# Kernel optimization log

Measured on AMD Instinct MI355X. Metric: run time of the kernel, lower is better.

The kernel has to match this reference:

```python
import jax, jax.numpy as jnp
import numpy as np

N_NODES = 100000
N_EDGES = 1600000
IN_CH = 165


def setup_inputs() -> dict:
    key = jax.random.key(0)
    ks = jax.random.split(key, 6)
    x = jax.random.normal(ks[0], (N_NODES, IN_CH), dtype=jnp.float32)
    edge_index = jax.random.randint(ks[1], (2, N_EDGES), 0, N_NODES, dtype=jnp.int32)
    # Glorot-ish init for weights
    W1 = jax.random.normal(ks[2], (IN_CH, 128), dtype=jnp.float32) * (1.0 / np.sqrt(IN_CH))
    b1 = jnp.zeros((128,), dtype=jnp.float32)
    W2 = jax.random.normal(ks[3], (128, 64), dtype=jnp.float32) * (1.0 / np.sqrt(128))
    b2 = jnp.zeros((64,), dtype=jnp.float32)
    Wo = jax.random.normal(ks[4], (64, 2), dtype=jnp.float32) * (1.0 / np.sqrt(64))
    bo = jnp.zeros((2,), dtype=jnp.float32)
    return {"x": x, "edge_index": edge_index, "W1": W1, "b1": b1,
            "W2": W2, "b2": b2, "Wo": Wo, "bo": bo}


def _gcn_norm(edge_index, n_nodes, dtype):
    """Add self-loops and compute symmetric normalization deg^-1/2 * deg^-1/2 (PyG gcn_norm)."""
    loops = jnp.arange(n_nodes, dtype=edge_index.dtype)
    ei = jnp.concatenate([edge_index, jnp.stack([loops, loops])], axis=1)
    row, col = ei[0], ei[1]
    deg = jax.ops.segment_sum(jnp.ones(ei.shape[1], dtype), col, num_segments=n_nodes)
    deg_inv_sqrt = jnp.where(deg > 0, jax.lax.rsqrt(deg), 0.0)
    norm = deg_inv_sqrt[row] * deg_inv_sqrt[col]  # [E+N]
    return row, col, norm


def _gcn_conv(h, row, col, norm, W, b, n_nodes):
    # transform first (F_in -> F_out), then gather-scale-scatter aggregate
    m = h @ W                                   # [N, F_out]
    msg = m[row] * norm[:, None]                # [E+N, F_out]
    agg = jax.ops.segment_sum(msg, col, num_segments=n_nodes)
    return agg + b


def reference(x, edge_index, W1, b1, W2, b2, Wo, bo):
    n_nodes = x.shape[0]
    row, col, norm = _gcn_norm(edge_index, n_nodes, x.dtype)
    h = jax.nn.relu(_gcn_conv(x, row, col, norm, W1, b1, n_nodes))
    h = jax.nn.relu(_gcn_conv(h, row, col, norm, W2, b2, n_nodes))
    return h @ Wo + bo  # [N, 2] logits
```

## Files before the change

kernel.cpp:

```cpp
#include <hip/hip_runtime.h>

#define N_NODES 100000
#define N_EDGES 1600000
#define IN_CH   165
#define BSHIFT 7
#define NBUCK  ((N_NODES + 127) / 128)
#define BCAP   3072
#define PA_BLOCKS 196
#define WSPLIT_BLOCKS 128
#define G1_BLOCKS ((N_NODES + 63) / 64)

typedef unsigned short ushort_t;
typedef _Float16 f16;
typedef _Float16 f16x8 __attribute__((ext_vector_type(8)));
typedef _Float16 hfrag8 __attribute__((ext_vector_type(8)));
typedef short bfrag8 __attribute__((ext_vector_type(8)));
typedef float f32x4 __attribute__((ext_vector_type(4)));

__device__ __forceinline__ ushort_t f2bf(float f) {
    unsigned u = __float_as_uint(f);
    unsigned r = (u + 0x7fffu + ((u >> 16) & 1u)) >> 16;
    return (ushort_t)r;
}
__device__ __forceinline__ float bf2f(ushort_t h) {
    return __uint_as_float(((unsigned)h) << 16);
}

__device__ __forceinline__ void fmix_lo(float& a, unsigned pair, float s) {
    asm("v_fma_mix_f32 %0, %1, %2, %0 op_sel_hi:[1,0,0]" : "+v"(a) : "v"(pair), "v"(s));
}
__device__ __forceinline__ void fmix_hi(float& a, unsigned pair, float s) {
    asm("v_fma_mix_f32 %0, %1, %2, %0 op_sel:[1,0,0] op_sel_hi:[1,0,0]" : "+v"(a) : "v"(pair), "v"(s));
}
__device__ __forceinline__ void fmix_acc8(float* acc, uint4 v, float s) {
    fmix_lo(acc[0], v.x, s); fmix_hi(acc[1], v.x, s);
    fmix_lo(acc[2], v.y, s); fmix_hi(acc[3], v.y, s);
    fmix_lo(acc[4], v.z, s); fmix_hi(acc[5], v.z, s);
    fmix_lo(acc[6], v.w, s); fmix_hi(acc[7], v.w, s);
}

__global__ void bucketA_kernel(const int* __restrict__ row, const int* __restrict__ col,
                               int* __restrict__ bfill, unsigned* __restrict__ tmp,
                               const float* __restrict__ W1, const float* __restrict__ W2,
                               ushort_t* __restrict__ wt1h, ushort_t* __restrict__ wt1l,
                               ushort_t* __restrict__ wt2h, ushort_t* __restrict__ wt2l) {
    __shared__ int lcnt[NBUCK];
    __shared__ int lcur[NBUCK];
    int t = threadIdx.x;
    if (blockIdx.x >= PA_BLOCKS) {
        int i = (blockIdx.x - PA_BLOCKS) * 256 + t;
        if (i < 128 * 192) {
            int ch = i / 192, k = i - ch * 192;
            float v = (k < IN_CH) ? W1[(size_t)k * 128 + ch] : 0.f;
            ushort_t h = f2bf(v);
            wt1h[i] = h;
            wt1l[i] = f2bf(v - bf2f(h));
        } else if (i < 128 * 192 + 64 * 128) {
            int j = i - 128 * 192;
            int ch = j / 128, k = j - ch * 128;
            float v = W2[(size_t)k * 64 + ch];
            f16 h = (f16)v;
            f16 l = (f16)(v - (float)h);
            wt2h[j] = *(ushort_t*)&h;
            wt2l[j] = *(ushort_t*)&l;
        }
        return;
    }
    int e0 = (int)((long)blockIdx.x * N_EDGES / PA_BLOCKS);
    int e1 = (int)((long)(blockIdx.x + 1) * N_EDGES / PA_BLOCKS);
    for (int i = t; i < NBUCK; i += 256) lcnt[i] = 0;
    __syncthreads();
    for (int e = e0 + t; e < e1; e += 256)
        atomicAdd(&lcnt[col[e] >> BSHIFT], 1);
    __syncthreads();
    for (int b = t; b < NBUCK; b += 256) {
        int c = lcnt[b];
        lcur[b] = (c > 0) ? (b * BCAP + atomicAdd(&bfill[b], c)) : 0;
    }
    __syncthreads();
    for (int e = e0 + t; e < e1; e += 256) {
        int cc = col[e];
        int b = cc >> BSHIFT;
        int p = atomicAdd(&lcur[b], 1);
        tmp[p] = ((unsigned)(cc & 127) << 17) | (unsigned)row[e];
    }
}

__launch_bounds__(256)
__global__ void g1prep_kernel(const unsigned* __restrict__ tmp, const int* __restrict__ bfill,
                              int* __restrict__ cnt, int* __restrict__ bbase, int* __restrict__ off,
                              const float* __restrict__ X,
                              const ushort_t* __restrict__ wth, const ushort_t* __restrict__ wtl,
                              f16* __restrict__ M, int n_nodes) {
    __shared__ char smem[20480];
    int t = threadIdx.x;
    if (blockIdx.x < NBUCK) {
        int* lcnt = (int*)smem;
        int* ssc  = (int*)(smem + 512);
        int b = blockIdx.x;
        if (t < 128) lcnt[t] = 0;
        __syncthreads();
        int total = min(bfill[b], BCAP);
        const unsigned* reg = tmp + (size_t)b * BCAP;
        for (int i = t; i < total; i += 256)
            atomicAdd(&lcnt[(reg[i] >> 17) & 127], 1);
        __syncthreads();
        if (t < 128) {
            int n = (b << BSHIFT) + t;
            if (n < N_NODES) cnt[n] = lcnt[t];
        }
        if (b == 0) {
            int v[4]; int run = 0;
            int base = t * 4;
            #pragma unroll
            for (int j = 0; j < 4; ++j) {
                int c = (base + j < NBUCK) ? bfill[base + j] : 0;
                v[j] = run; run += c;
            }
            ssc[t] = run;
            __syncthreads();
            for (int o = 1; o < 256; o <<= 1) {
                int x = (t >= o) ? ssc[t - o] : 0;
                __syncthreads();
                ssc[t] += x;
                __syncthreads();
            }
            int prev = (t > 0) ? ssc[t - 1] : 0;
            #pragma unroll
            for (int j = 0; j < 4; ++j)
                if (base + j < NBUCK) bbase[base + j] = prev + v[j];
            if (t == 0) off[N_NODES] = N_EDGES;
        }
        return;
    }
    constexpr int XP = 40;
    ushort_t (*wsh)[XP] = (ushort_t(*)[XP])smem;
    ushort_t (*wsl)[XP] = (ushort_t(*)[XP])(smem + 10240);

    int bid = blockIdx.x - NBUCK;
    int l = t & 63, wid = t >> 6;
    long node0 = (long)bid * 64;
    int r = (int)node0 + wid * 16 + (l & 15);
    int rr = min(r, n_nodes - 1);
    int q = l >> 4;
    const float* xrow = X + (size_t)rr * IN_CH;

    f32x4 acc[8];
    #pragma unroll
    for (int ct = 0; ct < 8; ++ct) acc[ct] = (f32x4){0.f, 0.f, 0.f, 0.f};

    bfrag8 wfh[2], wfl[2];
    float a[8];

    auto loadW = [&](int c) {
        int k0 = c * 32;
        #pragma unroll
        for (int i = 0; i < 2; ++i) {
            int idx = t + i * 256;
            int ch = idx >> 2, qq = idx & 3;
            wfh[i] = *(const bfrag8*)&wth[(size_t)ch * 192 + k0 + qq * 8];
            wfl[i] = *(const bfrag8*)&wtl[(size_t)ch * 192 + k0 + qq * 8];
        }
    };
    auto storeW = [&]() {
        #pragma unroll
        for (int i = 0; i < 2; ++i) {
            int idx = t + i * 256;
            int ch = idx >> 2, qq = idx & 3;
            *(bfrag8*)&wsh[ch][qq * 8] = wfh[i];
            *(bfrag8*)&wsl[ch][qq * 8] = wfl[i];
        }
    };
    auto loadX = [&](int c) {
        int k = c * 32 + q * 8;
        if (c < 5) {
            #pragma unroll
            for (int i = 0; i < 8; ++i) a[i] = xrow[k + i];
        } else {
            #pragma unroll
            for (int i = 0; i < 8; ++i) a[i] = 0.f;
            if (q == 0) {
                a[0] = xrow[160]; a[1] = xrow[161]; a[2] = xrow[162];
                a[3] = xrow[163]; a[4] = xrow[164];
            }
        }
    };

    loadW(0);
    loadX(0);
    #pragma unroll 1
    for (int c = 0; c < 6; ++c) {
        storeW();
        __syncthreads();
        if (c + 1 < 6) loadW(c + 1);
        bfrag8 ah, al;
        #pragma unroll
        for (int i = 0; i < 8; ++i) {
            ushort_t h = (ushort_t)(__float_as_uint(a[i]) >> 16);
            ah[i] = (short)h;
            al[i] = (short)f2bf(a[i] - bf2f(h));
        }
        if (c + 1 < 6) loadX(c + 1);
        #pragma unroll
        for (int ct = 0; ct < 8; ++ct) {
            bfrag8 bh = *(const bfrag8*)&wsh[ct * 16 + (l & 15)][q * 8];
            bfrag8 bl = *(const bfrag8*)&wsl[ct * 16 + (l & 15)][q * 8];
            acc[ct] = __builtin_amdgcn_mfma_f32_16x16x32_bf16(ah, bh, acc[ct], 0, 0, 0);
            acc[ct] = __builtin_amdgcn_mfma_f32_16x16x32_bf16(ah, bl, acc[ct], 0, 0, 0);
            acc[ct] = __builtin_amdgcn_mfma_f32_16x16x32_bf16(al, bh, acc[ct], 0, 0, 0);
        }
        __syncthreads();
    }

    int nl = wid * 16 + (l >> 4) * 4;
    #pragma unroll
    for (int ct = 0; ct < 8; ++ct) {
        int ch = ct * 16 + (l & 15);
        #pragma unroll
        for (int j = 0; j < 4; ++j) {
            long node = node0 + nl + j;
            if (node < n_nodes)
                M[node * 128 + ch] = (f16)acc[ct][j];
        }
    }
}

__global__ void bucketB2_kernel(const unsigned* __restrict__ tmp, const int* __restrict__ bfill,
                                const int* __restrict__ bbase, const int* __restrict__ cnt,
                                int* __restrict__ off, unsigned* __restrict__ srt) {
    __shared__ int sh[128];
    __shared__ int lcur[128];
    int b = blockIdx.x, t = threadIdx.x;
    int nb0 = b << BSHIFT;
    int base = bbase[b];
    if (t < 128) {
        int n = nb0 + t;
        sh[t] = (n < N_NODES) ? cnt[n] : 0;
    }
    __syncthreads();
    for (int o = 1; o < 128; o <<= 1) {
        int x = (t < 128 && t >= o) ? sh[t - o] : 0;
        __syncthreads();
        if (t < 128) sh[t] += x;
        __syncthreads();
    }
    if (t < 128) {
        int excl = (t > 0) ? sh[t - 1] : 0;
        int n = nb0 + t;
        if (n < N_NODES) off[n] = base + excl;
        lcur[t] = excl;
    }
    __syncthreads();
    int total = min(bfill[b], BCAP);
    const unsigned* reg = tmp + (size_t)b * BCAP;
    for (int i = t; i < total; i += 256) {
        unsigned e = reg[i];
        int c = (e >> 17) & 127;
        unsigned src = e & 0x1FFFFu;
        unsigned cs = min((unsigned)cnt[src], 255u);
        int p = atomicAdd(&lcur[c], 1);
        srt[base + p] = (cs << 17) | src;
    }
}

__launch_bounds__(256)
__global__ void gemm2_kernel(const f16* __restrict__ H,
                             const ushort_t* __restrict__ wth, const ushort_t* __restrict__ wtl,
                             f16* __restrict__ M, int n_nodes) {
    constexpr int XP = 40;
    __shared__ ushort_t wsh[64][XP];
    __shared__ ushort_t wsl[64][XP];
    int t = threadIdx.x;
    int l = t & 63, wid = t >> 6;
    long node0 = (long)blockIdx.x * 64;
    int r = (int)node0 + wid * 16 + (l & 15);
    int rr = min(r, n_nodes - 1);
    int q = l >> 4;
    const f16* hrow = H + (size_t)rr * 128;

    f32x4 acc[4];
    #pragma unroll
    for (int ct = 0; ct < 4; ++ct) acc[ct] = (f32x4){0.f, 0.f, 0.f, 0.f};

    bfrag8 wfh, wfl;
    auto loadW = [&](int c) {
        int ch = t >> 2, qq = t & 3;
        wfh = *(const bfrag8*)&wth[(size_t)ch * 128 + c * 32 + qq * 8];
        wfl = *(const bfrag8*)&wtl[(size_t)ch * 128 + c * 32 + qq * 8];
    };
    auto storeW = [&]() {
        int ch = t >> 2, qq = t & 3;
        *(bfrag8*)&wsh[ch][qq * 8] = wfh;
        *(bfrag8*)&wsl[ch][qq * 8] = wfl;
    };

    loadW(0);
    hfrag8 a = *(const hfrag8*)&hrow[q * 8];
    #pragma unroll 1
    for (int c = 0; c < 4; ++c) {
        storeW();
        __syncthreads();
        if (c + 1 < 4) loadW(c + 1);
        hfrag8 acur = a;
        if (c + 1 < 4) a = *(const hfrag8*)&hrow[(c + 1) * 32 + q * 8];
        #pragma unroll
        for (int ct = 0; ct < 4; ++ct) {
            hfrag8 bh = *(const hfrag8*)&wsh[ct * 16 + (l & 15)][q * 8];
            hfrag8 bl = *(const hfrag8*)&wsl[ct * 16 + (l & 15)][q * 8];
            acc[ct] = __builtin_amdgcn_mfma_f32_16x16x32_f16(acur, bh, acc[ct], 0, 0, 0);
            acc[ct] = __builtin_amdgcn_mfma_f32_16x16x32_f16(acur, bl, acc[ct], 0, 0, 0);
        }
        __syncthreads();
    }

    int nl = wid * 16 + (l >> 4) * 4;
    #pragma unroll
    for (int ct = 0; ct < 4; ++ct) {
        int ch = ct * 16 + (l & 15);
        #pragma unroll
        for (int j = 0; j < 4; ++j) {
            long node = node0 + nl + j;
            if (node < n_nodes)
                M[node * 64 + ch] = (f16)acc[ct][j];
        }
    }
}

__global__ void agg1_kernel(const f16* __restrict__ ms, const unsigned* __restrict__ srt,
                            const int* __restrict__ off,
                            const float* __restrict__ b1, f16* __restrict__ h1) {
    int wave = threadIdx.x >> 6;
    int lane = threadIdx.x & 63;
    int n = blockIdx.x * 4 + wave;
    if (n >= N_NODES) return;
    int g = lane >> 4, p = lane & 15;
    const char* msb = (const char*)ms;
    unsigned pb = (unsigned)p * 16;
    int s0 = off[n], s1 = off[n + 1];
    float dn = rsqrtf((float)(s1 - s0) + 1.f);
    float acc[8] = {0.f, 0.f, 0.f, 0.f, 0.f, 0.f, 0.f, 0.f};
    if (g == 0) {
        uint4 v = *(const uint4*)(msb + (unsigned)n * 256 + pb);
        fmix_acc8(acc, v, dn);
    }
    unsigned sv = (s0 + lane < s1) ? srt[s0 + lane] : 0;
    for (int base = s0; base < s1; base += 64) {
        int nb2 = base + 64;
        unsigned svn = (nb2 + lane < s1) ? srt[nb2 + lane] : 0;
        int cnt_ = min(64, s1 - base);
        int j = 0;
        for (; j + 15 < cnt_; j += 16) {
            unsigned e0 = (unsigned)__shfl((int)sv, j + g);
            unsigned e1 = (unsigned)__shfl((int)sv, j + 4 + g);
            unsigned e2 = (unsigned)__shfl((int)sv, j + 8 + g);
            unsigned e3 = (unsigned)__shfl((int)sv, j + 12 + g);
            uint4 v0 = *(const uint4*)(msb + (e0 & 0x1FFFFu) * 256 + pb);
            uint4 v1 = *(const uint4*)(msb + (e1 & 0x1FFFFu) * 256 + pb);
            uint4 v2 = *(const uint4*)(msb + (e2 & 0x1FFFFu) * 256 + pb);
            uint4 v3 = *(const uint4*)(msb + (e3 & 0x1FFFFu) * 256 + pb);
            float d0 = rsqrtf((float)(e0 >> 17) + 1.f);
            float d1 = rsqrtf((float)(e1 >> 17) + 1.f);
            float d2 = rsqrtf((float)(e2 >> 17) + 1.f);
            float d3 = rsqrtf((float)(e3 >> 17) + 1.f);
            fmix_acc8(acc, v0, d0);
            fmix_acc8(acc, v1, d1);
            fmix_acc8(acc, v2, d2);
            fmix_acc8(acc, v3, d3);
        }
        for (; j < cnt_; j += 4) {
            unsigned e = (unsigned)__shfl((int)sv, j + g);
            float ws = (j + g < cnt_) ? rsqrtf((float)(e >> 17) + 1.f) : 0.f;
            uint4 v = *(const uint4*)(msb + (e & 0x1FFFFu) * 256 + pb);
            fmix_acc8(acc, v, ws);
        }
        sv = svn;
    }
    #pragma unroll
    for (int i = 0; i < 8; ++i) {
        acc[i] += __shfl_xor(acc[i], 16);
        acc[i] += __shfl_xor(acc[i], 32);
    }
    if (lane < 16) {
        float4 ba = ((const float4*)b1)[lane * 2];
        float4 bb = ((const float4*)b1)[lane * 2 + 1];
        float bv[8] = {ba.x, ba.y, ba.z, ba.w, bb.x, bb.y, bb.z, bb.w};
        f16x8 r;
        #pragma unroll
        for (int i = 0; i < 8; ++i)
            r[i] = (f16)fmaxf(acc[i] * dn + bv[i], 0.f);
        *(f16x8*)(h1 + (size_t)n * 128 + lane * 8) = r;
    }
}

__global__ void agg2_kernel(const f16* __restrict__ ms, const unsigned* __restrict__ srt,
                            const int* __restrict__ off,
                            const float* __restrict__ b2, const float* __restrict__ Wo,
                            const float* __restrict__ bo, float* __restrict__ out) {
    int wave = threadIdx.x >> 6;
    int lane = threadIdx.x & 63;
    int n = blockIdx.x * 4 + wave;
    if (n >= N_NODES) return;
    int g = lane >> 3, p = lane & 7;
    const char* msb = (const char*)ms;
    unsigned pb = (unsigned)p * 16;
    int s0 = off[n], s1 = off[n + 1];
    float dn = rsqrtf((float)(s1 - s0) + 1.f);
    float acc[8] = {0.f, 0.f, 0.f, 0.f, 0.f, 0.f, 0.f, 0.f};
    if (g == 0) {
        uint4 v = *(const uint4*)(msb + (unsigned)n * 128 + pb);
        fmix_acc8(acc, v, dn);
    }
    unsigned sv = (s0 + lane < s1) ? srt[s0 + lane] : 0;
    for (int base = s0; base < s1; base += 64) {
        int nb2 = base + 64;
        unsigned svn = (nb2 + lane < s1) ? srt[nb2 + lane] : 0;
        int cnt_ = min(64, s1 - base);
        int j = 0;
        for (; j + 15 < cnt_; j += 16) {
            unsigned e0 = (unsigned)__shfl((int)sv, j + g);
            unsigned e1 = (unsigned)__shfl((int)sv, j + 8 + g);
            uint4 v0 = *(const uint4*)(msb + (e0 & 0x1FFFFu) * 128 + pb);
            uint4 v1 = *(const uint4*)(msb + (e1 & 0x1FFFFu) * 128 + pb);
            float d0 = rsqrtf((float)(e0 >> 17) + 1.f);
            float d1 = rsqrtf((float)(e1 >> 17) + 1.f);
            fmix_acc8(acc, v0, d0);
            fmix_acc8(acc, v1, d1);
        }
        for (; j < cnt_; j += 8) {
            unsigned e = (unsigned)__shfl((int)sv, j + g);
            float ws = (j + g < cnt_) ? rsqrtf((float)(e >> 17) + 1.f) : 0.f;
            uint4 v = *(const uint4*)(msb + (e & 0x1FFFFu) * 128 + pb);
            fmix_acc8(acc, v, ws);
        }
        sv = svn;
    }
    #pragma unroll
    for (int i = 0; i < 8; ++i) {
        acc[i] += __shfl_xor(acc[i], 8);
        acc[i] += __shfl_xor(acc[i], 16);
        acc[i] += __shfl_xor(acc[i], 32);
    }
    float p0 = 0.f, p1 = 0.f;
    #pragma unroll
    for (int i = 0; i < 8; ++i) {
        int ch = p * 8 + i;
        float hc = fmaxf(acc[i] * dn + b2[ch], 0.f);
        p0 = fmaf(hc, Wo[ch * 2], p0);
        p1 = fmaf(hc, Wo[ch * 2 + 1], p1);
    }
    p0 += __shfl_xor(p0, 1); p1 += __shfl_xor(p1, 1);
    p0 += __shfl_xor(p0, 2); p1 += __shfl_xor(p1, 2);
    p0 += __shfl_xor(p0, 4); p1 += __shfl_xor(p1, 4);
    if (lane == 0) {
        out[(size_t)n * 2]     = p0 + bo[0];
        out[(size_t)n * 2 + 1] = p1 + bo[1];
    }
}

extern "C" void kernel_launch(void* const* d_in, const int* in_sizes, int n_in,
                              void* d_out, int out_size, void* d_ws, size_t ws_size,
                              hipStream_t stream) {
    const float* x  = (const float*)d_in[0];
    const int*   ei = (const int*)d_in[1];
    const int*   row = ei;
    const int*   col = ei + N_EDGES;
    const float* W1 = (const float*)d_in[2];
    const float* b1 = (const float*)d_in[3];
    const float* W2 = (const float*)d_in[4];
    const float* b2 = (const float*)d_in[5];
    const float* Wo = (const float*)d_in[6];
    const float* bo = (const float*)d_in[7];
    float* out = (float*)d_out;

    char* base = (char*)d_ws;
    auto alloc = [&](size_t bytes) {
        char* p = base;
        base += (bytes + 255) & ~(size_t)255;
        return p;
    };
    int*      cnt  = (int*)alloc((size_t)N_NODES * 4);
    int*      off  = (int*)alloc((size_t)(N_NODES + 1) * 4);
    int*      bbase= (int*)alloc((size_t)(NBUCK + 1) * 4);
    int*      bfill= (int*)alloc((size_t)NBUCK * 4);
    unsigned* tmp  = (unsigned*)alloc((size_t)NBUCK * BCAP * 4 + 4096);
    unsigned* srt  = (unsigned*)alloc((size_t)N_EDGES * 4);
    f16*      m    = (f16*)alloc((size_t)N_NODES * 128 * 2);
    f16*      h1   = (f16*)alloc((size_t)N_NODES * 128 * 2);
    ushort_t* wt1h = (ushort_t*)alloc((size_t)128 * 192 * 2);
    ushort_t* wt1l = (ushort_t*)alloc((size_t)128 * 192 * 2);
    ushort_t* wt2h = (ushort_t*)alloc((size_t)64 * 128 * 2);
    ushort_t* wt2l = (ushort_t*)alloc((size_t)64 * 128 * 2);

    hipMemsetAsync(bfill, 0, (size_t)NBUCK * 4, stream);

    bucketA_kernel<<<PA_BLOCKS + WSPLIT_BLOCKS, 256, 0, stream>>>(
        row, col, bfill, tmp, W1, W2, wt1h, wt1l, wt2h, wt2l);

    g1prep_kernel<<<NBUCK + G1_BLOCKS, 256, 0, stream>>>(
        tmp, bfill, cnt, bbase, off, x, wt1h, wt1l, m, N_NODES);

    bucketB2_kernel<<<NBUCK, 256, 0, stream>>>(tmp, bfill, bbase, cnt, off, srt);

    agg1_kernel<<<(N_NODES + 3) / 4, 256, 0, stream>>>(m, srt, off, b1, h1);

    gemm2_kernel<<<G1_BLOCKS, 256, 0, stream>>>(h1, wt2h, wt2l, m, N_NODES);
    agg2_kernel<<<(N_NODES + 3) / 4, 256, 0, stream>>>(m, srt, off, b2, Wo, bo, out);
}
```

Baseline: 219.2 us.

## Fuse CSR scatter into bucket prep kernel and precompute deg^-1/2 table

Removes the separate bucketB2 launch by having each bucket block compute its own global base via a prefix reduction over bfill, then do the local scan and scatter of source ids into srt in the same kernel as the first GEMM. Degree normalisation is now stored once as a per-node float table read by the aggregation kernels, replacing the packed in-edge count and rsqrt in srt entries. It also raises the bucketing block count. The cost is a redundant O(NBUCK) prefix sum per bucket block and an extra gather of dis[src] per edge in the aggregations.

```diff
diff --git a/kernel.cpp b/kernel.cpp
--- a/kernel.cpp
+++ b/kernel.cpp
@@ -6,7 +6,7 @@
 #define BSHIFT 7
 #define NBUCK  ((N_NODES + 127) / 128)
 #define BCAP   3072
-#define PA_BLOCKS 196
+#define PA_BLOCKS 256
 #define WSPLIT_BLOCKS 128
 #define G1_BLOCKS ((N_NODES + 63) / 64)
 
@@ -87,16 +87,20 @@
 }
 
 __launch_bounds__(256)
-__global__ void g1prep_kernel(const unsigned* __restrict__ tmp, const int* __restrict__ bfill,
-                              int* __restrict__ cnt, int* __restrict__ bbase, int* __restrict__ off,
-                              const float* __restrict__ X,
-                              const ushort_t* __restrict__ wth, const ushort_t* __restrict__ wtl,
-                              f16* __restrict__ M, int n_nodes) {
+__global__ void b2g1_kernel(const unsigned* __restrict__ tmp, const int* __restrict__ bfill,
+                            float* __restrict__ dis, int* __restrict__ off,
+                            unsigned* __restrict__ srt,
+                            const float* __restrict__ X,
+                            const ushort_t* __restrict__ wth, const ushort_t* __restrict__ wtl,
+                            f16* __restrict__ M, int n_nodes) {
     __shared__ char smem[20480];
     int t = threadIdx.x;
+    int lane = t & 63, wid = t >> 6;
     if (blockIdx.x < NBUCK) {
         int* lcnt = (int*)smem;
-        int* ssc  = (int*)(smem + 512);
+        int* wred = (int*)(smem + 512);
+        int* sh   = (int*)(smem + 1024);
+        int* lcur = (int*)(smem + 1536);
         int b = blockIdx.x;
         if (t < 128) lcnt[t] = 0;
         __syncthreads();
@@ -104,32 +108,40 @@
         const unsigned* reg = tmp + (size_t)b * BCAP;
         for (int i = t; i < total; i += 256)
             atomicAdd(&lcnt[(reg[i] >> 17) & 127], 1);
-        __syncthreads();
+        int s = 0;
+        for (int j = t; j < b; j += 256) s += bfill[j];
+        #pragma unroll
+        for (int o = 32; o > 0; o >>= 1) s += __shfl_xor(s, o);
+        if (lane == 0) wred[wid] = s;
+        __syncthreads();
+        int base = wred[0] + wred[1] + wred[2] + wred[3];
+        int myc = 0;
         if (t < 128) {
+            myc = lcnt[t];
             int n = (b << BSHIFT) + t;
-            if (n < N_NODES) cnt[n] = lcnt[t];
-        }
-        if (b == 0) {
-            int v[4]; int run = 0;
-            int base = t * 4;
-            #pragma unroll
-            for (int j = 0; j < 4; ++j) {
-                int c = (base + j < NBUCK) ? bfill[base + j] : 0;
-                v[j] = run; run += c;
-            }
-            ssc[t] = run;
+            if (n < N_NODES) dis[n] = rsqrtf((float)(myc + 1));
+            sh[t] = myc;
+        }
+        __syncthreads();
+        for (int o = 1; o < 128; o <<= 1) {
+            int x = (t < 128 && t >= o) ? sh[t - o] : 0;
             __syncthreads();
-            for (int o = 1; o < 256; o <<= 1) {
-                int x = (t >= o) ? ssc[t - o] : 0;
-                __syncthreads();
-                ssc[t] += x;
-                __syncthreads();
-            }
-            int prev = (t > 0) ? ssc[t - 1] : 0;
-            #pragma unroll
-            for (int j = 0; j < 4; ++j)
-                if (base + j < NBUCK) bbase[base + j] = prev + v[j];
-            if (t == 0) off[N_NODES] = N_EDGES;
+            if (t < 128) sh[t] += x;
+            __syncthreads();
+        }
+        if (t < 128) {
+            int excl = sh[t] - myc;
+            int n = (b << BSHIFT) + t;
+            if (n < N_NODES) off[n] = base + excl;
+            lcur[t] = excl;
+        }
+        if (b == 0 && t == 0) off[N_NODES] = N_EDGES;
+        __syncthreads();
+        for (int i = t; i < total; i += 256) {
+            unsigned e = reg[i];
+            int c = (e >> 17) & 127;
+            int p = atomicAdd(&lcur[c], 1);
+            srt[base + p] = e & 0x1FFFFu;
         }
         return;
     }
@@ -138,11 +150,10 @@
     ushort_t (*wsl)[XP] = (ushort_t(*)[XP])(smem + 10240);
 
     int bid = blockIdx.x - NBUCK;
-    int l = t & 63, wid = t >> 6;
     long node0 = (long)bid * 64;
-    int r = (int)node0 + wid * 16 + (l & 15);
+    int r = (int)node0 + wid * 16 + (lane & 15);
     int rr = min(r, n_nodes - 1);
-    int q = l >> 4;
+    int q = lane >> 4;
     const float* xrow = X + (size_t)rr * IN_CH;
 
     f32x4 acc[8];
@@ -203,8 +214,8 @@
         if (c + 1 < 6) loadX(c + 1);
         #pragma unroll
         for (int ct = 0; ct < 8; ++ct) {
-            bfrag8 bh = *(const bfrag8*)&wsh[ct * 16 + (l & 15)][q * 8];
-            bfrag8 bl = *(const bfrag8*)&wsl[ct * 16 + (l & 15)][q * 8];
+            bfrag8 bh = *(const bfrag8*)&wsh[ct * 16 + (lane & 15)][q * 8];
+            bfrag8 bl = *(const bfrag8*)&wsl[ct * 16 + (lane & 15)][q * 8];
             acc[ct] = __builtin_amdgcn_mfma_f32_16x16x32_bf16(ah, bh, acc[ct], 0, 0, 0);
             acc[ct] = __builtin_amdgcn_mfma_f32_16x16x32_bf16(ah, bl, acc[ct], 0, 0, 0);
             acc[ct] = __builtin_amdgcn_mfma_f32_16x16x32_bf16(al, bh, acc[ct], 0, 0, 0);
@@ -212,54 +223,16 @@
         __syncthreads();
     }
 
-    int nl = wid * 16 + (l >> 4) * 4;
+    int nl = wid * 16 + (lane >> 4) * 4;
     #pragma unroll
     for (int ct = 0; ct < 8; ++ct) {
-        int ch = ct * 16 + (l & 15);
+        int ch = ct * 16 + (lane & 15);
         #pragma unroll
         for (int j = 0; j < 4; ++j) {
             long node = node0 + nl + j;
             if (node < n_nodes)
                 M[node * 128 + ch] = (f16)acc[ct][j];
         }
-    }
-}
-
-__global__ void bucketB2_kernel(const unsigned* __restrict__ tmp, const int* __restrict__ bfill,
-                                const int* __restrict__ bbase, const int* __restrict__ cnt,
-                                int* __restrict__ off, unsigned* __restrict__ srt) {
-    __shared__ int sh[128];
-    __shared__ int lcur[128];
-    int b = blockIdx.x, t = threadIdx.x;
-    int nb0 = b << BSHIFT;
-    int base = bbase[b];
-    if (t < 128) {
-        int n = nb0 + t;
-        sh[t] = (n < N_NODES) ? cnt[n] : 0;
-    }
-    __syncthreads();
-    for (int o = 1; o < 128; o <<= 1) {
-        int x = (t < 128 && t >= o) ? sh[t - o] : 0;
-        __syncthreads();
-        if (t < 128) sh[t] += x;
-        __syncthreads();
-    }
-    if (t < 128) {
-        int excl = (t > 0) ? sh[t - 1] : 0;
-        int n = nb0 + t;
-        if (n < N_NODES) off[n] = base + excl;
-        lcur[t] = excl;
-    }
-    __syncthreads();
-    int total = min(bfill[b], BCAP);
-    const unsigned* reg = tmp + (size_t)b * BCAP;
-    for (int i = t; i < total; i += 256) {
-        unsigned e = reg[i];
-        int c = (e >> 17) & 127;
-        unsigned src = e & 0x1FFFFu;
-        unsigned cs = min((unsigned)cnt[src], 255u);
-        int p = atomicAdd(&lcur[c], 1);
-        srt[base + p] = (cs << 17) | src;
     }
 }
 
@@ -327,7 +300,7 @@
 }
 
 __global__ void agg1_kernel(const f16* __restrict__ ms, const unsigned* __restrict__ srt,
-                            const int* __restrict__ off,
+                            const int* __restrict__ off, const float* __restrict__ dis,
                             const float* __restrict__ b1, f16* __restrict__ h1) {
     int wave = threadIdx.x >> 6;
     int lane = threadIdx.x & 63;
@@ -354,14 +327,14 @@
             unsigned e1 = (unsigned)__shfl((int)sv, j + 4 + g);
             unsigned e2 = (unsigned)__shfl((int)sv, j + 8 + g);
             unsigned e3 = (unsigned)__shfl((int)sv, j + 12 + g);
-            uint4 v0 = *(const uint4*)(msb + (e0 & 0x1FFFFu) * 256 + pb);
-            uint4 v1 = *(const uint4*)(msb + (e1 & 0x1FFFFu) * 256 + pb);
-            uint4 v2 = *(const uint4*)(msb + (e2 & 0x1FFFFu) * 256 + pb);
-            uint4 v3 = *(const uint4*)(msb + (e3 & 0x1FFFFu) * 256 + pb);
-            float d0 = rsqrtf((float)(e0 >> 17) + 1.f);
-            float d1 = rsqrtf((float)(e1 >> 17) + 1.f);
-            float d2 = rsqrtf((float)(e2 >> 17) + 1.f);
-            float d3 = rsqrtf((float)(e3 >> 17) + 1.f);
+            uint4 v0 = *(const uint4*)(msb + e0 * 256 + pb);
+            uint4 v1 = *(const uint4*)(msb + e1 * 256 + pb);
+            uint4 v2 = *(const uint4*)(msb + e2 * 256 + pb);
+            uint4 v3 = *(const uint4*)(msb + e3 * 256 + pb);
+            float d0 = dis[e0];
+            float d1 = dis[e1];
+            float d2 = dis[e2];
+            float d3 = dis[e3];
             fmix_acc8(acc, v0, d0);
             fmix_acc8(acc, v1, d1);
             fmix_acc8(acc, v2, d2);
@@ -369,8 +342,8 @@
         }
         for (; j < cnt_; j += 4) {
             unsigned e = (unsigned)__shfl((int)sv, j + g);
-            float ws = (j + g < cnt_) ? rsqrtf((float)(e >> 17) + 1.f) : 0.f;
-            uint4 v = *(const uint4*)(msb + (e & 0x1FFFFu) * 256 + pb);
+            float ws = (j + g < cnt_) ? dis[e] : 0.f;
+            uint4 v = *(const uint4*)(msb + e * 256 + pb);
             fmix_acc8(acc, v, ws);
         }
         sv = svn;
@@ -393,7 +366,7 @@
 }
 
 __global__ void agg2_kernel(const f16* __restrict__ ms, const unsigned* __restrict__ srt,
-                            const int* __restrict__ off,
+                            const int* __restrict__ off, const float* __restrict__ dis,
                             const float* __restrict__ b2, const float* __restrict__ Wo,
                             const float* __restrict__ bo, float* __restrict__ out) {
     int wave = threadIdx.x >> 6;
@@ -419,17 +392,17 @@
         for (; j + 15 < cnt_; j += 16) {
             unsigned e0 = (unsigned)__shfl((int)sv, j + g);
             unsigned e1 = (unsigned)__shfl((int)sv, j + 8 + g);
-            uint4 v0 = *(const uint4*)(msb + (e0 & 0x1FFFFu) * 128 + pb);
-            uint4 v1 = *(const uint4*)(msb + (e1 & 0x1FFFFu) * 128 + pb);
-            float d0 = rsqrtf((float)(e0 >> 17) + 1.f);
-            float d1 = rsqrtf((float)(e1 >> 17) + 1.f);
+            uint4 v0 = *(const uint4*)(msb + e0 * 128 + pb);
+            uint4 v1 = *(const uint4*)(msb + e1 * 128 + pb);
+            float d0 = dis[e0];
+            float d1 = dis[e1];
             fmix_acc8(acc, v0, d0);
             fmix_acc8(acc, v1, d1);
         }
         for (; j < cnt_; j += 8) {
             unsigned e = (unsigned)__shfl((int)sv, j + g);
-            float ws = (j + g < cnt_) ? rsqrtf((float)(e >> 17) + 1.f) : 0.f;
-            uint4 v = *(const uint4*)(msb + (e & 0x1FFFFu) * 128 + pb);
+            float ws = (j + g < cnt_) ? dis[e] : 0.f;
+            uint4 v = *(const uint4*)(msb + e * 128 + pb);
             fmix_acc8(acc, v, ws);
         }
         sv = svn;
@@ -478,9 +451,8 @@
         base += (bytes + 255) & ~(size_t)255;
         return p;
     };
-    int*      cnt  = (int*)alloc((size_t)N_NODES * 4);
+    float*    dis  = (float*)alloc((size_t)N_NODES * 4);
     int*      off  = (int*)alloc((size_t)(N_NODES + 1) * 4);
-    int*      bbase= (int*)alloc((size_t)(NBUCK + 1) * 4);
     int*      bfill= (int*)alloc((size_t)NBUCK * 4);
     unsigned* tmp  = (unsigned*)alloc((size_t)NBUCK * BCAP * 4 + 4096);
     unsigned* srt  = (unsigned*)alloc((size_t)N_EDGES * 4);
@@ -496,13 +468,11 @@
     bucketA_kernel<<<PA_BLOCKS + WSPLIT_BLOCKS, 256, 0, stream>>>(
         row, col, bfill, tmp, W1, W2, wt1h, wt1l, wt2h, wt2l);
 
-    g1prep_kernel<<<NBUCK + G1_BLOCKS, 256, 0, stream>>>(
-        tmp, bfill, cnt, bbase, off, x, wt1h, wt1l, m, N_NODES);
-
-    bucketB2_kernel<<<NBUCK, 256, 0, stream>>>(tmp, bfill, bbase, cnt, off, srt);
-
-    agg1_kernel<<<(N_NODES + 3) / 4, 256, 0, stream>>>(m, srt, off, b1, h1);
+    b2g1_kernel<<<NBUCK + G1_BLOCKS, 256, 0, stream>>>(
+        tmp, bfill, dis, off, srt, x, wt1h, wt1l, m, N_NODES);
+
+    agg1_kernel<<<(N_NODES + 3) / 4, 256, 0, stream>>>(m, srt, off, dis, b1, h1);
 
     gemm2_kernel<<<G1_BLOCKS, 256, 0, stream>>>(h1, wt2h, wt2l, m, N_NODES);
-    agg2_kernel<<<(N_NODES + 3) / 4, 256, 0, stream>>>(m, srt, off, b2, Wo, bo, out);
-}
+    agg2_kernel<<<(N_NODES + 3) / 4, 256, 0, stream>>>(m, srt, off, dis, b2, Wo, bo, out);
+}
```

Result: faster. 209.5 us (-4.4%).
